# Kernel optimization log

Hardware: AMD Instinct MI355X
Metric: run time of the kernel (lower is better)

The kernel has to match this reference:

```python
import jax, jax.numpy as jnp
import numpy as np

B, L, D, E, K, DFF = 2, 2048, 1024, 8, 2, 4096


def setup_inputs() -> dict:
    key = jax.random.key(0)
    kx, kr, kg, ku, kd = jax.random.split(key, 5)
    scale = 0.02
    return {
        "x": jax.random.normal(kx, (B, L, D), dtype=jnp.float32),
        "Wr": jax.random.normal(kr, (E, D), dtype=jnp.float32) * scale,   # router: logits = x @ Wr.T
        "Wg": jax.random.normal(kg, (E, DFF, D), dtype=jnp.float32) * scale,  # gate proj per expert
        "Wu": jax.random.normal(ku, (E, DFF, D), dtype=jnp.float32) * scale,  # up proj per expert
        "Wd": jax.random.normal(kd, (E, D, DFF), dtype=jnp.float32) * scale,  # down proj per expert
    }


def reference(x, Wr, Wg, Wu, Wd):
    Bb, Ll, Dd = x.shape
    T = Bb * Ll
    xt = x.reshape(T, Dd)                                   # [T, D]
    logits = jnp.einsum("td,ed->te", xt, Wr)                # router logits [T, E]
    scores = jax.nn.softmax(logits, axis=-1)
    k_scores, k_ids = jax.lax.top_k(scores, K)              # [T, K]
    eps = jnp.finfo(x.dtype).eps
    k_w = k_scores / (k_scores.sum(axis=-1, keepdims=True) + eps)  # renormalized top-k weights
    # combine[t, e] = sum_k k_w[t, k] * (k_ids[t, k] == e)
    combine = jnp.sum(jax.nn.one_hot(k_ids, E, dtype=x.dtype) * k_w[..., None], axis=1)  # [T, E]
    # GluMLP per expert, computed densely over all tokens (reference form)
    g = jnp.einsum("td,efd->etf", xt, Wg)                   # [E, T, DFF]
    u = jnp.einsum("td,efd->etf", xt, Wu)                   # [E, T, DFF]
    h = jax.nn.relu(g) * u
    out_e = jnp.einsum("etf,edf->etd", h, Wd)               # [E, T, D]
    out = jnp.einsum("te,etd->td", combine, out_e)          # weighted combine [T, D]
    return out.reshape(Bb, Ll, Dd)
```

## Files before the change

kernel.cpp:

```cpp
#include <hip/hip_runtime.h>
#include <hip/hip_bf16.h>

#define Tt 4096
#define Dd 1024
#define Ee 8
#define Kk 2
#define Ff 4096

using f32x4  = __attribute__((ext_vector_type(4))) float;
using bf16x8 = __attribute__((ext_vector_type(8))) short;

__device__ __forceinline__ unsigned short f2bf(float f) {
    union { float fp; unsigned int u; } v; v.fp = f;
    unsigned int u = v.u;
    return (unsigned short)((u + 0x7FFFu + ((u >> 16) & 1u)) >> 16);
}

__device__ __forceinline__ void gl16(const void* g, void* l) {
    __builtin_amdgcn_global_load_lds(
        (const __attribute__((address_space(1))) void*)g,
        (__attribute__((address_space(3))) void*)l, 16, 0, 0);
}

__global__ void router_kernel(const float* __restrict__ x, const float* __restrict__ Wr,
                              int* __restrict__ ids, float* __restrict__ wts,
                              int* __restrict__ counts) {
    const int t = blockIdx.x;
    const int lane = threadIdx.x;
    const float* xr = x + (size_t)t * Dd;
    float xv[16];
#pragma unroll
    for (int i = 0; i < 16; ++i) xv[i] = xr[lane + 64 * i];
    double dot[Ee];
#pragma unroll
    for (int e = 0; e < Ee; ++e) {
        const float* wr = Wr + e * Dd;
        double s = 0.0;
#pragma unroll
        for (int i = 0; i < 16; ++i) s += (double)xv[i] * (double)wr[lane + 64 * i];
        dot[e] = s;
    }
#pragma unroll
    for (int off = 32; off >= 1; off >>= 1) {
#pragma unroll
        for (int e = 0; e < Ee; ++e) dot[e] += __shfl_xor(dot[e], off, 64);
    }
    if (lane == 0) {
        float lg[Ee];
#pragma unroll
        for (int e = 0; e < Ee; ++e) lg[e] = (float)dot[e];
        float m = lg[0];
        for (int e = 1; e < Ee; ++e) m = fmaxf(m, lg[e]);
        float ex[Ee]; float sum = 0.f;
        for (int e = 0; e < Ee; ++e) { ex[e] = expf(lg[e] - m); sum += ex[e]; }
        float s0 = -1.f, s1 = -1.f; int i0 = 0, i1 = 0;
        for (int e = 0; e < Ee; ++e) {
            float s = ex[e];
            if (s > s0)      { s1 = s0; i1 = i0; s0 = s; i0 = e; }
            else if (s > s1) { s1 = s; i1 = e; }
        }
        float inv = 1.f / sum;
        float sc0 = s0 * inv, sc1 = s1 * inv;
        float den = sc0 + sc1 + 1.1920929e-7f;
        ids[2 * t] = i0; ids[2 * t + 1] = i1;
        wts[2 * t] = sc0 / den; wts[2 * t + 1] = sc1 / den;
        atomicAdd(&counts[i0], 1);
        atomicAdd(&counts[i1], 1);
    }
}

__global__ void cvtw_kernel(const float* __restrict__ src, unsigned short* __restrict__ dst) {
    size_t i = ((size_t)blockIdx.x * blockDim.x + threadIdx.x) * 8;
    float4 a = *(const float4*)(src + i);
    float4 b = *(const float4*)(src + i + 4);
    uint4 o;
    o.x = (unsigned)f2bf(a.x) | ((unsigned)f2bf(a.y) << 16);
    o.y = (unsigned)f2bf(a.z) | ((unsigned)f2bf(a.w) << 16);
    o.z = (unsigned)f2bf(b.x) | ((unsigned)f2bf(b.y) << 16);
    o.w = (unsigned)f2bf(b.z) | ((unsigned)f2bf(b.w) << 16);
    *(uint4*)(dst + i) = o;
}

__global__ void cvt_wgu_kernel(const float* __restrict__ Wg, const float* __restrict__ Wu,
                               unsigned short* __restrict__ Wgu) {
    size_t tid = (size_t)blockIdx.x * blockDim.x + threadIdx.x;
    size_t row = tid >> 7;
    int dc  = (int)(tid & 127);
    int e   = (int)(row >> 13);
    int j   = (int)(row & 8191);
    int fg = j >> 5, s = (j >> 4) & 1, fi = j & 15;
    int f  = fg * 16 + fi;
    const float* src = (s ? Wu : Wg) + ((size_t)e * Ff + f) * Dd + dc * 8;
    float4 a = *(const float4*)(src);
    float4 b = *(const float4*)(src + 4);
    uint4 o;
    o.x = (unsigned)f2bf(a.x) | ((unsigned)f2bf(a.y) << 16);
    o.y = (unsigned)f2bf(a.z) | ((unsigned)f2bf(a.w) << 16);
    o.z = (unsigned)f2bf(b.x) | ((unsigned)f2bf(b.y) << 16);
    o.w = (unsigned)f2bf(b.z) | ((unsigned)f2bf(b.w) << 16);
    *(uint4*)(Wgu + row * Dd + dc * 8) = o;
}

__global__ void scan_kernel(const int* __restrict__ counts, int* __restrict__ cursor,
                            int* __restrict__ eoff) {
    if (threadIdx.x == 0) {
        int acc = 0;
        for (int e = 0; e < Ee; ++e) { eoff[e] = acc; cursor[e] = acc; acc += counts[e]; }
        eoff[Ee] = acc;
    }
}

__global__ void scatter_kernel(const int* __restrict__ ids, const float* __restrict__ wts,
                               int* __restrict__ cursor, int* __restrict__ rows,
                               float* __restrict__ roww) {
    int t = blockIdx.x * blockDim.x + threadIdx.x;
    if (t >= Tt) return;
#pragma unroll
    for (int k = 0; k < Kk; ++k) {
        int e = ids[2 * t + k];
        int pos = atomicAdd(&cursor[e], 1);
        rows[pos] = t;
        roww[pos] = wts[2 * t + k];
    }
}


#define MFMA_BF16(a, b, c) __builtin_amdgcn_mfma_f32_16x16x32_bf16(a, b, c, 0, 0, 0)

template<bool G2>
__launch_bounds__(512, 1)
__global__ void gemm_8ph(const unsigned short* __restrict__ Abase,
                         const unsigned short* __restrict__ Bbase,
                         const int* __restrict__ eoff, const int* __restrict__ rows,
                         const float* __restrict__ roww,
                         unsigned short* __restrict__ H,
                         float* __restrict__ out) {
    constexpr int KLEN = G2 ? Ff : Dd;
    constexpr int NT   = KLEN / 64;
    const int e   = blockIdx.z;
    const int off = eoff[e];
    const int ne  = eoff[e + 1] - off;
    const int m0  = blockIdx.y * 256;
    if (m0 >= ne) return;
    const int n0  = blockIdx.x * 256;

    __shared__ __align__(16) unsigned short L[65536];
    unsigned short* Ls = L;

    const int tid  = threadIdx.x;
    const int lane = tid & 63;
    const int w    = tid >> 6;
    const int wr   = w >> 2;
    const int wc   = w & 3;
    const int lr   = lane & 15;
    const int lc   = lane >> 4;

    const int sr = lane >> 3;
    const int cA = (lane & 7) ^ sr;
    int asrc[4];
#pragma unroll
    for (int qq = 0; qq < 4; ++qq) {
        int rr = m0 + qq * 64 + w * 8 + sr;
        if (rr > ne - 1) rr = ne - 1;
        asrc[qq] = (G2 ? (off + rr) : rows[off + rr]) * KLEN + cA * 8;
    }
    const unsigned short* Bp = Bbase + (size_t)e * (G2 ? (size_t)Dd * Ff : (size_t)8192 * Dd);
    int bsrc[4];
#pragma unroll
    for (int qq = 0; qq < 4; ++qq) {
        int rN = n0 + qq * 64 + w * 8 + sr;
        bsrc[qq] = rN * KLEN + cA * 8;
    }

#define STAGE_A(T, Hh) { const int bo_ = ((T) & 1) * 32768; const int kt_ = (T) * 64;            \
    gl16(Abase + asrc[2*(Hh)]   + kt_, Ls + bo_ + (2*(Hh))   * 4096 + w * 512);                  \
    gl16(Abase + asrc[2*(Hh)+1] + kt_, Ls + bo_ + (2*(Hh)+1) * 4096 + w * 512); }
#define STAGE_B(T, Hh) { const int bo_ = ((T) & 1) * 32768 + 16384; const int kt_ = (T) * 64;    \
    gl16(Bp + bsrc[2*(Hh)]   + kt_, Ls + bo_ + (2*(Hh))   * 4096 + w * 512);                     \
    gl16(Bp + bsrc[2*(Hh)+1] + kt_, Ls + bo_ + (2*(Hh)+1) * 4096 + w * 512); }

    const int ccx0 = ((0 * 4 + lc) ^ (lr & 7)) * 8;
    const int ccx1 = ((1 * 4 + lc) ^ (lr & 7)) * 8;
    const int aB = wr * 8192 + lr * 64;
    const int bB = 16384 + (wc >> 1) * 8192 + (wc & 1) * 4096 + lr * 64;

    f32x4 acc[8][4];
#pragma unroll
    for (int m = 0; m < 8; ++m)
#pragma unroll
        for (int n = 0; n < 4; ++n) acc[m][n] = (f32x4){0.f, 0.f, 0.f, 0.f};

    STAGE_A(0, 0); STAGE_A(0, 1); STAGE_B(0, 0); STAGE_B(0, 1);
    STAGE_A(1, 0); STAGE_A(1, 1);
    asm volatile("s_waitcnt vmcnt(4)" ::: "memory");
    __builtin_amdgcn_sched_barrier(0);
    __builtin_amdgcn_s_barrier();

    bf16x8 a0[8], a1[8], b0[4], b1[4];

    for (int t = 0; t < NT; ++t) {
        const int bo = (t & 1) * 32768;
#pragma unroll
        for (int m = 0; m < 8; ++m) a0[m] = *(const bf16x8*)(Ls + bo + aB + m * 1024 + ccx0);
#pragma unroll
        for (int n = 0; n < 4; ++n) b0[n] = *(const bf16x8*)(Ls + bo + bB + n * 1024 + ccx0);
        if (t + 1 < NT) STAGE_B(t + 1, 0);
        __builtin_amdgcn_s_barrier();
        asm volatile("s_waitcnt lgkmcnt(0)" ::: "memory");
        __builtin_amdgcn_sched_barrier(0);
        __builtin_amdgcn_s_setprio(1);
#pragma unroll
        for (int m = 0; m < 8; ++m) {
            acc[m][0] = MFMA_BF16(a0[m], b0[0], acc[m][0]);
            acc[m][1] = MFMA_BF16(a0[m], b0[1], acc[m][1]);
        }
        __builtin_amdgcn_s_setprio(0);
        __builtin_amdgcn_s_barrier();
#pragma unroll
        for (int m = 0; m < 8; ++m) a1[m] = *(const bf16x8*)(Ls + bo + aB + m * 1024 + ccx1);
        if (t + 1 < NT) STAGE_B(t + 1, 1);
        __builtin_amdgcn_s_barrier();
        __builtin_amdgcn_s_setprio(1);
#pragma unroll
        for (int m = 0; m < 8; ++m) {
            acc[m][2] = MFMA_BF16(a0[m], b0[2], acc[m][2]);
            acc[m][3] = MFMA_BF16(a0[m], b0[3], acc[m][3]);
        }
        __builtin_amdgcn_s_setprio(0);
        asm volatile("s_waitcnt lgkmcnt(0)" ::: "memory");
        __builtin_amdgcn_sched_barrier(0);
        __builtin_amdgcn_s_barrier();
#pragma unroll
        for (int n = 0; n < 4; ++n) b1[n] = *(const bf16x8*)(Ls + bo + bB + n * 1024 + ccx1);
        if (t + 2 < NT) STAGE_A(t + 2, 0);
        __builtin_amdgcn_s_barrier();
        asm volatile("s_waitcnt lgkmcnt(0)" ::: "memory");
        __builtin_amdgcn_sched_barrier(0);
        __builtin_amdgcn_s_setprio(1);
#pragma unroll
        for (int m = 0; m < 8; ++m) {
            acc[m][0] = MFMA_BF16(a1[m], b1[0], acc[m][0]);
            acc[m][1] = MFMA_BF16(a1[m], b1[1], acc[m][1]);
        }
        __builtin_amdgcn_s_setprio(0);
        __builtin_amdgcn_s_barrier();
        if (t + 2 < NT) STAGE_A(t + 2, 1);
        __builtin_amdgcn_s_setprio(1);
#pragma unroll
        for (int m = 0; m < 8; ++m) {
            acc[m][2] = MFMA_BF16(a1[m], b1[2], acc[m][2]);
            acc[m][3] = MFMA_BF16(a1[m], b1[3], acc[m][3]);
        }
        __builtin_amdgcn_s_setprio(0);
        if (t + 2 < NT) { asm volatile("s_waitcnt vmcnt(4)" ::: "memory"); }
        else            { asm volatile("s_waitcnt vmcnt(0)" ::: "memory"); }
        __builtin_amdgcn_sched_barrier(0);
        __builtin_amdgcn_s_barrier();
    }

    if constexpr (!G2) {
        const int fg16 = ((n0 + wc * 64) >> 5) * 16 + lr;
#pragma unroll
        for (int m = 0; m < 8; ++m) {
            const int itok = m0 + wr * 128 + m * 16 + (lane >> 4) * 4;
#pragma unroll
            for (int r = 0; r < 4; ++r) {
                const int i = itok + r;
                if (i < ne) {
                    unsigned short* hp = H + (size_t)(off + i) * Ff;
#pragma unroll
                    for (int np = 0; np < 2; ++np) {
                        const float g = acc[m][2 * np][r];
                        const float u = acc[m][2 * np + 1][r];
                        hp[fg16 + np * 16] = f2bf(fmaxf(g, 0.f) * u);
                    }
                }
            }
        }
    } else {
        const int dbase = n0 + wc * 64;
#pragma unroll
        for (int m = 0; m < 8; ++m) {
            const int ib = m0 + wr * 128 + m * 16 + (lane >> 4) * 4;
#pragma unroll
            for (int r = 0; r < 4; ++r) {
                const int i = ib + r;
                if (i < ne) {
                    const int   t  = rows[off + i];
                    const float wg = roww[off + i];
                    float* op = out + (size_t)t * Dd + dbase + lr;
#pragma unroll
                    for (int n = 0; n < 4; ++n)
                        atomicAdd(&op[n * 16], wg * acc[m][n][r]);
                }
            }
        }
    }
#undef STAGE_A
#undef STAGE_B
}

extern "C" void kernel_launch(void* const* d_in, const int* in_sizes, int n_in,
                              void* d_out, int out_size, void* d_ws, size_t ws_size,
                              hipStream_t stream) {
    const float* x  = (const float*)d_in[0];
    const float* Wr = (const float*)d_in[1];
    const float* Wg = (const float*)d_in[2];
    const float* Wu = (const float*)d_in[3];
    const float* Wd = (const float*)d_in[4];
    float* out = (float*)d_out;
    char* ws = (char*)d_ws;

    const size_t WELEM    = (size_t)Ee * Ff * Dd;
    const size_t OFF_IDS  = 256;
    const size_t OFF_WTS  = OFF_IDS  + (size_t)Tt * 2 * 4;
    const size_t OFF_ROWS = OFF_WTS  + (size_t)Tt * 2 * 4;
    const size_t OFF_ROWW = OFF_ROWS + (size_t)Tt * Kk * 4;
    const size_t OFF_XB   = OFF_ROWW + (size_t)Tt * Kk * 4;
    const size_t OFF_H    = OFF_XB   + (size_t)Tt * Dd * 2;
    const size_t OFF_WGU  = OFF_H    + (size_t)Tt * Kk * Ff * 2;
    const size_t OFF_WD   = OFF_WGU  + WELEM * 2 * 2;
    const size_t NEED     = OFF_WD   + WELEM * 2;
    if (ws_size < NEED) return;

    int* counts = (int*)ws;
    int* cursor = (int*)(ws + 32);
    int* eoff   = (int*)(ws + 64);
    int* ids    = (int*)(ws + OFF_IDS);
    float* wts  = (float*)(ws + OFF_WTS);
    int* rows   = (int*)(ws + OFF_ROWS);
    float* roww = (float*)(ws + OFF_ROWW);
    unsigned short* xb  = (unsigned short*)(ws + OFF_XB);
    unsigned short* H   = (unsigned short*)(ws + OFF_H);
    unsigned short* Wgu = (unsigned short*)(ws + OFF_WGU);
    unsigned short* Wdb = (unsigned short*)(ws + OFF_WD);

    hipMemsetAsync(ws, 0, 256, stream);
    hipMemsetAsync(d_out, 0, (size_t)Tt * Dd * 4, stream);

    router_kernel  <<<Tt, 64, 0, stream>>>(x, Wr, ids, wts, counts);
    cvtw_kernel    <<<(Tt * Dd / 8) / 256, 256, 0, stream>>>(x, xb);
    scan_kernel    <<<1, 64, 0, stream>>>(counts, cursor, eoff);
    scatter_kernel <<<Tt / 256, 256, 0, stream>>>(ids, wts, cursor, rows, roww);

    cvt_wgu_kernel <<<(int)(WELEM * 2 / 8 / 256), 256, 0, stream>>>(Wg, Wu, Wgu);
    cvtw_kernel    <<<(int)(WELEM / 8 / 256), 256, 0, stream>>>(Wd, Wdb);

    gemm_8ph<false><<<dim3(2 * Ff / 256, Tt / 256, Ee), 512, 0, stream>>>(
        xb, Wgu, eoff, rows, roww, H, out);
    gemm_8ph<true> <<<dim3(Dd / 256, Tt / 256, Ee), 512, 0, stream>>>(
        H, Wdb, eoff, rows, roww, H, out);
}
```

Before: 515.0 us.

## Split-K the down-projection GEMM and replace output atomics with a weighted reduce

The down-projection GEMM now splits its K dimension in two, doubling the number of workgroups. Each workgroup writes plain stores into a per-(token,k) partial buffer, reusing the bf16 weight workspace region, instead of doing weighted atomicAdds into the output. A new reduce kernel then applies the routing weights and sums the partials, which also removes the output memset. Separately, the conversion of x to bf16 is folded into the router kernel, dropping one launch and one read of x. The cost is an extra pass over a 64MB partial buffer.

```diff
diff --git a/kernel.cpp b/kernel.cpp
--- a/kernel.cpp
+++ b/kernel.cpp
@@ -24,20 +24,33 @@
 
 __global__ void router_kernel(const float* __restrict__ x, const float* __restrict__ Wr,
                               int* __restrict__ ids, float* __restrict__ wts,
-                              int* __restrict__ counts) {
+                              int* __restrict__ counts, unsigned short* __restrict__ xb) {
     const int t = blockIdx.x;
     const int lane = threadIdx.x;
-    const float* xr = x + (size_t)t * Dd;
+    const float* xr = x + (size_t)t * Dd + lane * 16;
     float xv[16];
 #pragma unroll
-    for (int i = 0; i < 16; ++i) xv[i] = xr[lane + 64 * i];
+    for (int i = 0; i < 4; ++i) *(float4*)(xv + 4 * i) = *(const float4*)(xr + 4 * i);
+    uint4 o0, o1;
+    o0.x = (unsigned)f2bf(xv[0])  | ((unsigned)f2bf(xv[1])  << 16);
+    o0.y = (unsigned)f2bf(xv[2])  | ((unsigned)f2bf(xv[3])  << 16);
+    o0.z = (unsigned)f2bf(xv[4])  | ((unsigned)f2bf(xv[5])  << 16);
+    o0.w = (unsigned)f2bf(xv[6])  | ((unsigned)f2bf(xv[7])  << 16);
+    o1.x = (unsigned)f2bf(xv[8])  | ((unsigned)f2bf(xv[9])  << 16);
+    o1.y = (unsigned)f2bf(xv[10]) | ((unsigned)f2bf(xv[11]) << 16);
+    o1.z = (unsigned)f2bf(xv[12]) | ((unsigned)f2bf(xv[13]) << 16);
+    o1.w = (unsigned)f2bf(xv[14]) | ((unsigned)f2bf(xv[15]) << 16);
+    unsigned short* xo = xb + (size_t)t * Dd + lane * 16;
+    *(uint4*)(xo) = o0;
+    *(uint4*)(xo + 8) = o1;
+
     double dot[Ee];
 #pragma unroll
     for (int e = 0; e < Ee; ++e) {
-        const float* wr = Wr + e * Dd;
+        const float* wr = Wr + e * Dd + lane * 16;
         double s = 0.0;
 #pragma unroll
-        for (int i = 0; i < 16; ++i) s += (double)xv[i] * (double)wr[lane + 64 * i];
+        for (int i = 0; i < 16; ++i) s += (double)xv[i] * (double)wr[i];
         dot[e] = s;
     }
 #pragma unroll
@@ -110,17 +123,15 @@
     }
 }
 
-__global__ void scatter_kernel(const int* __restrict__ ids, const float* __restrict__ wts,
-                               int* __restrict__ cursor, int* __restrict__ rows,
-                               float* __restrict__ roww) {
+__global__ void scatter_kernel(const int* __restrict__ ids,
+                               int* __restrict__ cursor, int* __restrict__ rows) {
     int t = blockIdx.x * blockDim.x + threadIdx.x;
     if (t >= Tt) return;
 #pragma unroll
     for (int k = 0; k < Kk; ++k) {
         int e = ids[2 * t + k];
         int pos = atomicAdd(&cursor[e], 1);
-        rows[pos] = t;
-        roww[pos] = wts[2 * t + k];
+        rows[pos] = 2 * t + k;
     }
 }
 
@@ -132,20 +143,21 @@
 __global__ void gemm_8ph(const unsigned short* __restrict__ Abase,
                          const unsigned short* __restrict__ Bbase,
                          const int* __restrict__ eoff, const int* __restrict__ rows,
-                         const float* __restrict__ roww,
                          unsigned short* __restrict__ H,
-                         float* __restrict__ out) {
+                         float* __restrict__ partial) {
     constexpr int KLEN = G2 ? Ff : Dd;
-    constexpr int NT   = KLEN / 64;
+    constexpr int NT   = (G2 ? 2048 : 1024) / 64;
     const int e   = blockIdx.z;
     const int off = eoff[e];
     const int ne  = eoff[e + 1] - off;
-    const int m0  = blockIdx.y * 256;
+    const int my  = G2 ? (blockIdx.y >> 1) : blockIdx.y;
+    const int sK  = G2 ? (blockIdx.y & 1) : 0;
+    const int koff = sK * 2048;
+    const int m0  = my * 256;
     if (m0 >= ne) return;
     const int n0  = blockIdx.x * 256;
 
-    __shared__ __align__(16) unsigned short L[65536];
-    unsigned short* Ls = L;
+    __shared__ __align__(16) unsigned short Ls[65536];
 
     const int tid  = threadIdx.x;
     const int lane = tid & 63;
@@ -162,7 +174,7 @@
     for (int qq = 0; qq < 4; ++qq) {
         int rr = m0 + qq * 64 + w * 8 + sr;
         if (rr > ne - 1) rr = ne - 1;
-        asrc[qq] = (G2 ? (off + rr) : rows[off + rr]) * KLEN + cA * 8;
+        asrc[qq] = (G2 ? (off + rr) : (rows[off + rr] >> 1)) * KLEN + cA * 8;
     }
     const unsigned short* Bp = Bbase + (size_t)e * (G2 ? (size_t)Dd * Ff : (size_t)8192 * Dd);
     int bsrc[4];
@@ -172,17 +184,21 @@
         bsrc[qq] = rN * KLEN + cA * 8;
     }
 
-#define STAGE_A(T, Hh) { const int bo_ = ((T) & 1) * 32768; const int kt_ = (T) * 64;            \
-    gl16(Abase + asrc[2*(Hh)]   + kt_, Ls + bo_ + (2*(Hh))   * 4096 + w * 512);                  \
-    gl16(Abase + asrc[2*(Hh)+1] + kt_, Ls + bo_ + (2*(Hh)+1) * 4096 + w * 512); }
-#define STAGE_B(T, Hh) { const int bo_ = ((T) & 1) * 32768 + 16384; const int kt_ = (T) * 64;    \
-    gl16(Bp + bsrc[2*(Hh)]   + kt_, Ls + bo_ + (2*(Hh))   * 4096 + w * 512);                     \
-    gl16(Bp + bsrc[2*(Hh)+1] + kt_, Ls + bo_ + (2*(Hh)+1) * 4096 + w * 512); }
+    auto STAGE_A = [&](int T, int Hh) {
+        const int bo_ = (T & 1) * 32768; const int kt_ = koff + T * 64;
+        gl16(Abase + asrc[2 * Hh]     + kt_, Ls + bo_ + (2 * Hh)     * 4096 + w * 512);
+        gl16(Abase + asrc[2 * Hh + 1] + kt_, Ls + bo_ + (2 * Hh + 1) * 4096 + w * 512);
+    };
+    auto STAGE_B = [&](int T, int Hh) {
+        const int bo_ = (T & 1) * 32768 + 16384; const int kt_ = koff + T * 64;
+        gl16(Bp + bsrc[2 * Hh]     + kt_, Ls + bo_ + (2 * Hh)     * 4096 + w * 512);
+        gl16(Bp + bsrc[2 * Hh + 1] + kt_, Ls + bo_ + (2 * Hh + 1) * 4096 + w * 512);
+    };
 
     const int ccx0 = ((0 * 4 + lc) ^ (lr & 7)) * 8;
     const int ccx1 = ((1 * 4 + lc) ^ (lr & 7)) * 8;
     const int aB = wr * 8192 + lr * 64;
-    const int bB = 16384 + (wc >> 1) * 8192 + (wc & 1) * 4096 + lr * 64;
+    const int bB = 16384 + wc * 4096 + lr * 64;
 
     f32x4 acc[8][4];
 #pragma unroll
@@ -286,18 +302,33 @@
             for (int r = 0; r < 4; ++r) {
                 const int i = ib + r;
                 if (i < ne) {
-                    const int   t  = rows[off + i];
-                    const float wg = roww[off + i];
-                    float* op = out + (size_t)t * Dd + dbase + lr;
-#pragma unroll
-                    for (int n = 0; n < 4; ++n)
-                        atomicAdd(&op[n * 16], wg * acc[m][n][r]);
+                    const int tr = rows[off + i];
+                    float* op = partial + ((size_t)sK * 8192 + tr) * Dd + dbase + lr;
+#pragma unroll
+                    for (int n = 0; n < 4; ++n) op[n * 16] = acc[m][n][r];
                 }
             }
         }
     }
-#undef STAGE_A
-#undef STAGE_B
+}
+
+__global__ void reduce_kernel(const float* __restrict__ P, const float* __restrict__ wts,
+                              float* __restrict__ out) {
+    const size_t idx = (size_t)blockIdx.x * blockDim.x + threadIdx.x;
+    const size_t t  = idx >> 8;
+    const int   dq  = (int)(idx & 255);
+    const float w0 = wts[2 * t], w1 = wts[2 * t + 1];
+    const float4* p00 = (const float4*)(P + (2 * t)        * Dd) + dq;
+    const float4* p01 = (const float4*)(P + (2 * t + 1)    * Dd) + dq;
+    const float4* p10 = (const float4*)(P + ((size_t)8192 + 2 * t)     * Dd) + dq;
+    const float4* p11 = (const float4*)(P + ((size_t)8192 + 2 * t + 1) * Dd) + dq;
+    float4 a = *p00, b = *p01, c = *p10, d = *p11;
+    float4 o;
+    o.x = w0 * (a.x + c.x) + w1 * (b.x + d.x);
+    o.y = w0 * (a.y + c.y) + w1 * (b.y + d.y);
+    o.z = w0 * (a.z + c.z) + w1 * (b.z + d.z);
+    o.w = w0 * (a.w + c.w) + w1 * (b.w + d.w);
+    ((float4*)(out + t * Dd))[dq] = o;
 }
 
 extern "C" void kernel_launch(void* const* d_in, const int* in_sizes, int n_in,
@@ -329,25 +360,25 @@
     int* ids    = (int*)(ws + OFF_IDS);
     float* wts  = (float*)(ws + OFF_WTS);
     int* rows   = (int*)(ws + OFF_ROWS);
-    float* roww = (float*)(ws + OFF_ROWW);
     unsigned short* xb  = (unsigned short*)(ws + OFF_XB);
     unsigned short* H   = (unsigned short*)(ws + OFF_H);
     unsigned short* Wgu = (unsigned short*)(ws + OFF_WGU);
     unsigned short* Wdb = (unsigned short*)(ws + OFF_WD);
+    float* partial = (float*)(ws + OFF_WGU);
 
     hipMemsetAsync(ws, 0, 256, stream);
-    hipMemsetAsync(d_out, 0, (size_t)Tt * Dd * 4, stream);
-
-    router_kernel  <<<Tt, 64, 0, stream>>>(x, Wr, ids, wts, counts);
-    cvtw_kernel    <<<(Tt * Dd / 8) / 256, 256, 0, stream>>>(x, xb);
+
+    router_kernel  <<<Tt, 64, 0, stream>>>(x, Wr, ids, wts, counts, xb);
     scan_kernel    <<<1, 64, 0, stream>>>(counts, cursor, eoff);
-    scatter_kernel <<<Tt / 256, 256, 0, stream>>>(ids, wts, cursor, rows, roww);
+    scatter_kernel <<<Tt / 256, 256, 0, stream>>>(ids, cursor, rows);
 
     cvt_wgu_kernel <<<(int)(WELEM * 2 / 8 / 256), 256, 0, stream>>>(Wg, Wu, Wgu);
     cvtw_kernel    <<<(int)(WELEM / 8 / 256), 256, 0, stream>>>(Wd, Wdb);
 
     gemm_8ph<false><<<dim3(2 * Ff / 256, Tt / 256, Ee), 512, 0, stream>>>(
-        xb, Wgu, eoff, rows, roww, H, out);
-    gemm_8ph<true> <<<dim3(Dd / 256, Tt / 256, Ee), 512, 0, stream>>>(
-        H, Wdb, eoff, rows, roww, H, out);
-}
+        xb, Wgu, eoff, rows, H, partial);
+    gemm_8ph<true> <<<dim3(Dd / 256, 2 * (Tt / 256), Ee), 512, 0, stream>>>(
+        H, Wdb, eoff, rows, H, partial);
+
+    reduce_kernel  <<<(Tt * Dd / 4) / 256, 256, 0, stream>>>(partial, wts, out);
+}
```

Result: no change. 517.7 us (+0.5%).
